# Kernel tuning notes

Hardware: AMD Instinct MI355X
Metric: run time of the kernel (lower is better)

Reference implementation:

```python
import jax, jax.numpy as jnp
import numpy as np

T = 8  # number of tables; all include_last_offsets=True


def setup_inputs() -> dict:
    key = jax.random.key(0)
    ks = jax.random.split(key, 3 * T)
    N = 2097152   # indices per table
    B = 8192      # batch per table; offsets length B+1 (include_last_offset)
    VOCAB = 1000000
    inp = {}
    for i in range(T):
        inp[f"indices_{i}"] = jax.random.randint(ks[i], (N,), 0, VOCAB, dtype=jnp.int32)
        off = jnp.sort(jax.random.randint(ks[T + i], (B + 1,), 0, N, dtype=jnp.int32))
        inp[f"offsets_{i}"] = off
        inp[f"weights_{i}"] = jax.random.uniform(ks[2 * T + i], (N,), dtype=jnp.float32)
    return inp


def reference(indices_0, indices_1, indices_2, indices_3, indices_4, indices_5, indices_6, indices_7,
              offsets_0, offsets_1, offsets_2, offsets_3, offsets_4, offsets_5, offsets_6, offsets_7,
              weights_0, weights_1, weights_2, weights_3, weights_4, weights_5, weights_6, weights_7):
    indices_list = [indices_0, indices_1, indices_2, indices_3, indices_4, indices_5, indices_6, indices_7]
    offsets_list = [offsets_0, offsets_1, offsets_2, offsets_3, offsets_4, offsets_5, offsets_6, offsets_7]
    weights_list = [weights_0, weights_1, weights_2, weights_3, weights_4, weights_5, weights_6, weights_7]

    sizes = [x.shape[0] for x in indices_list]
    # offsets_accs: static prefix sums of per-table index counts (offset rebasing)
    accs = np.concatenate([[0], np.cumsum(sizes)]).astype(np.int32)

    combined_indices = jnp.concatenate(indices_list).astype(jnp.int32)
    # include_last_offset=True for all tables: take first len-1 entries per table,
    # rebase by accumulated index count, then append grand total.
    combined_offsets = jnp.concatenate(
        [off[:-1] + jnp.int32(accs[i]) for i, off in enumerate(offsets_list)]
        + [jnp.array([accs[-1]], dtype=jnp.int32)]
    )
    per_sample_weights = jnp.concatenate(weights_list)
    return combined_indices, combined_offsets, per_sample_weights
```

## Files before the change

### kernel.cpp

```cpp
#include <hip/hip_runtime.h>

#define T_TABLES  8
#define N_TAB     2097152
#define B_TAB     8192
#define NV_TAB    (N_TAB / 4)
#define LOG2_NV   19
#define LOG2_NTAB 21
#define LOG2_B    13

#define TOTAL_IDX (T_TABLES * N_TAB)
#define N_OFF_OUT (T_TABLES * B_TAB + 1)
#define NTHREADS  2097152
#define WPB       2048

struct TablePtrs {
    const int*   idx[T_TABLES];
    const int*   off[T_TABLES];
    const float* wgt[T_TABLES];
};

typedef float __attribute__((ext_vector_type(4))) float4v;
typedef int   __attribute__((ext_vector_type(4))) int4v;

__global__ __launch_bounds__(256)
void tbe_prep_kernel(TablePtrs p, float* __restrict__ out) {
    __shared__ float lds[WPB];

    float* __restrict__ out_idx = out;
    float* __restrict__ out_off = out + TOTAL_IDX;
    float* __restrict__ out_w   = out + TOTAL_IDX + N_OFF_OUT;

    const int tid = blockIdx.x * blockDim.x + threadIdx.x;
    const int i   = threadIdx.x;

    const int v0 = tid;
    const int v1 = tid + NTHREADS;
    const int t0 = v0 >> LOG2_NV, j0 = (v0 & (NV_TAB - 1)) << 2;
    const int t1 = v1 >> LOG2_NV, j1 = (v1 & (NV_TAB - 1)) << 2;
    const int4v ia = __builtin_nontemporal_load((const int4v*)(p.idx[t0] + j0));
    const int4v ib = __builtin_nontemporal_load((const int4v*)(p.idx[t1] + j1));

    const int    D0   = blockIdx.x * WPB;
    const int    tw   = D0 >> LOG2_NTAB;
    const int    jw   = D0 & (N_TAB - 1);
    const float* wsrc = p.wgt[tw] + jw;
    const float4v wa = __builtin_nontemporal_load((const float4v*)(wsrc + 4 * i));
    const float4v wb = __builtin_nontemporal_load((const float4v*)(wsrc + 4 * (i + 256)));

    *(float4v*)(lds + 4 * i)         = wa;
    *(float4v*)(lds + 4 * (i + 256)) = wb;

    float4v oa, ob;
    oa[0] = (float)ia[0]; oa[1] = (float)ia[1]; oa[2] = (float)ia[2]; oa[3] = (float)ia[3];
    ob[0] = (float)ib[0]; ob[1] = (float)ib[1]; ob[2] = (float)ib[2]; ob[3] = (float)ib[3];
    __builtin_nontemporal_store(oa, (float4v*)(out_idx + (v0 << 2)));
    __builtin_nontemporal_store(ob, (float4v*)(out_idx + (v1 << 2)));

    if (tid < T_TABLES * B_TAB) {
        const int t = tid >> LOG2_B;
        const int k = tid & (B_TAB - 1);
        out_off[tid] = (float)(p.off[t][k] + t * N_TAB);
    } else if (tid == T_TABLES * B_TAB) {
        out_off[tid] = (float)TOTAL_IDX;
    }

    __syncthreads();

    float* __restrict__ wdst = out_w + D0;
    {
        const int c = i;
        float4v s;
        s[0] = lds[3 + 4 * c]; s[1] = lds[4 + 4 * c];
        s[2] = lds[5 + 4 * c]; s[3] = lds[6 + 4 * c];
        __builtin_nontemporal_store(s, (float4v*)(wdst + 3 + 4 * c));
    }
    if (i < 255) {
        const int c = i + 256;
        float4v s;
        s[0] = lds[3 + 4 * c]; s[1] = lds[4 + 4 * c];
        s[2] = lds[5 + 4 * c]; s[3] = lds[6 + 4 * c];
        __builtin_nontemporal_store(s, (float4v*)(wdst + 3 + 4 * c));
    } else {
        wdst[0]       = lds[0];
        wdst[1]       = lds[1];
        wdst[2]       = lds[2];
        wdst[WPB - 1] = lds[WPB - 1];
    }
}

extern "C" void kernel_launch(void* const* d_in, const int* in_sizes, int n_in,
                              void* d_out, int out_size, void* d_ws, size_t ws_size,
                              hipStream_t stream) {
    TablePtrs p;
    const bool interleaved = (n_in >= 2 && in_sizes[1] == B_TAB + 1);
    for (int i = 0; i < T_TABLES; ++i) {
        if (interleaved) {
            p.idx[i] = (const int*)  d_in[3 * i + 0];
            p.off[i] = (const int*)  d_in[3 * i + 1];
            p.wgt[i] = (const float*)d_in[3 * i + 2];
        } else {
            p.idx[i] = (const int*)  d_in[i];
            p.off[i] = (const int*)  d_in[T_TABLES + i];
            p.wgt[i] = (const float*)d_in[2 * T_TABLES + i];
        }
    }
    float* out = (float*)d_out;

    dim3 grid(8192), block(256);
    hipLaunchKernelGGL(tbe_prep_kernel, grid, block, 0, stream, p, out);
}
```

Baseline: 260.1 us.

## Split fused prep kernel into separate index-convert and weight-shift kernels

Splits the single fused kernel into two launches: one converts indices to float with a contiguous per-block chunk layout, and one handles the weight shift through LDS plus the offsets. The index access pattern also changes from a grid-strided two-half split to contiguous 2048-element blocks. The aim is simpler, more streaming-friendly memory access per kernel. It adds a second launch, and the two kernels no longer overlap their traffic within a block.

```diff
diff --git a/kernel.cpp b/kernel.cpp
--- a/kernel.cpp
+++ b/kernel.cpp
@@ -3,14 +3,11 @@
 #define T_TABLES  8
 #define N_TAB     2097152
 #define B_TAB     8192
-#define NV_TAB    (N_TAB / 4)
-#define LOG2_NV   19
 #define LOG2_NTAB 21
 #define LOG2_B    13
 
 #define TOTAL_IDX (T_TABLES * N_TAB)
 #define N_OFF_OUT (T_TABLES * B_TAB + 1)
-#define NTHREADS  2097152
 #define WPB       2048
 
 struct TablePtrs {
@@ -23,38 +20,44 @@
 typedef int   __attribute__((ext_vector_type(4))) int4v;
 
 __global__ __launch_bounds__(256)
-void tbe_prep_kernel(TablePtrs p, float* __restrict__ out) {
+void tbe_idx_kernel(TablePtrs p, float* __restrict__ out) {
+    const int i  = threadIdx.x;
+    const int D0 = blockIdx.x * WPB;
+    const int t  = D0 >> LOG2_NTAB;
+    const int j  = D0 & (N_TAB - 1);
+    const int* __restrict__ src = p.idx[t] + j;
+    float*     __restrict__ dst = out + D0;
+
+    const int4v ia = __builtin_nontemporal_load((const int4v*)(src + 4 * i));
+    const int4v ib = __builtin_nontemporal_load((const int4v*)(src + 4 * (i + 256)));
+
+    float4v oa, ob;
+    oa[0] = (float)ia[0]; oa[1] = (float)ia[1]; oa[2] = (float)ia[2]; oa[3] = (float)ia[3];
+    ob[0] = (float)ib[0]; ob[1] = (float)ib[1]; ob[2] = (float)ib[2]; ob[3] = (float)ib[3];
+
+    __builtin_nontemporal_store(oa, (float4v*)(dst + 4 * i));
+    __builtin_nontemporal_store(ob, (float4v*)(dst + 4 * (i + 256)));
+}
+
+__global__ __launch_bounds__(256)
+void tbe_wgt_kernel(TablePtrs p, float* __restrict__ out) {
     __shared__ float lds[WPB];
 
-    float* __restrict__ out_idx = out;
     float* __restrict__ out_off = out + TOTAL_IDX;
     float* __restrict__ out_w   = out + TOTAL_IDX + N_OFF_OUT;
 
     const int tid = blockIdx.x * blockDim.x + threadIdx.x;
     const int i   = threadIdx.x;
 
-    const int v0 = tid;
-    const int v1 = tid + NTHREADS;
-    const int t0 = v0 >> LOG2_NV, j0 = (v0 & (NV_TAB - 1)) << 2;
-    const int t1 = v1 >> LOG2_NV, j1 = (v1 & (NV_TAB - 1)) << 2;
-    const int4v ia = __builtin_nontemporal_load((const int4v*)(p.idx[t0] + j0));
-    const int4v ib = __builtin_nontemporal_load((const int4v*)(p.idx[t1] + j1));
-
     const int    D0   = blockIdx.x * WPB;
     const int    tw   = D0 >> LOG2_NTAB;
     const int    jw   = D0 & (N_TAB - 1);
-    const float* wsrc = p.wgt[tw] + jw;
+    const float* __restrict__ wsrc = p.wgt[tw] + jw;
     const float4v wa = __builtin_nontemporal_load((const float4v*)(wsrc + 4 * i));
     const float4v wb = __builtin_nontemporal_load((const float4v*)(wsrc + 4 * (i + 256)));
 
     *(float4v*)(lds + 4 * i)         = wa;
     *(float4v*)(lds + 4 * (i + 256)) = wb;
-
-    float4v oa, ob;
-    oa[0] = (float)ia[0]; oa[1] = (float)ia[1]; oa[2] = (float)ia[2]; oa[3] = (float)ia[3];
-    ob[0] = (float)ib[0]; ob[1] = (float)ib[1]; ob[2] = (float)ib[2]; ob[3] = (float)ib[3];
-    __builtin_nontemporal_store(oa, (float4v*)(out_idx + (v0 << 2)));
-    __builtin_nontemporal_store(ob, (float4v*)(out_idx + (v1 << 2)));
 
     if (tid < T_TABLES * B_TAB) {
         const int t = tid >> LOG2_B;
@@ -107,5 +110,6 @@
     float* out = (float*)d_out;
 
     dim3 grid(8192), block(256);
-    hipLaunchKernelGGL(tbe_prep_kernel, grid, block, 0, stream, p, out);
+    hipLaunchKernelGGL(tbe_idx_kernel, grid, block, 0, stream, p, out);
+    hipLaunchKernelGGL(tbe_wgt_kernel, grid, block, 0, stream, p, out);
 }
```

Result: no change. 261.5 us (+0.5%).
